# Optimization experiments

Hardware: AMD Instinct MI355X
Metric: run time of the kernel (lower is better)

Reference implementation:

```python
import jax, jax.numpy as jnp
import numpy as np

REG = 0.01
NUM_ITER = 5


def _l2norm(x):
    return x / jnp.linalg.norm(x, axis=-1, keepdims=True)


def setup_inputs() -> dict:
    key = jax.random.key(0)
    k1, k2 = jax.random.split(key)
    B, D = 8192, 256
    img = _l2norm(jax.random.normal(k1, (B, D), dtype=jnp.float32))
    # correlate text with image so diagonal similarity ~1 (CLIP-like), keeping
    # K = exp(-(1-sim)/0.01) numerically meaningful
    txt = _l2norm(img + 0.1 * jax.random.normal(k2, (B, D), dtype=jnp.float32))
    labels = jnp.arange(B, dtype=jnp.int64)
    logit_scale = jnp.float32(100.0)  # unused by the module, kept for signature
    return {"all_image_features": img, "all_text_features": txt,
            "logit_scale": logit_scale, "labels": labels}


def _sinkhorn_loss(M, labels, reg=REG, num_iter=NUM_ITER):
    n = M.shape[0]
    b_val = jnp.asarray(1.0 / n, M.dtype)  # b = [1/n, ...]; a = ones -> Kp = K
    u0 = jnp.ones((n,), M.dtype) / n
    v0 = jnp.ones((n,), M.dtype) / n
    K = jnp.exp(M / -reg)  # [n, n]

    def body(carry, _):
        u, v, done = carry
        KtU = K.T @ u                       # [n]
        v_new = b_val / KtU
        u_new = 1.0 / (K @ v_new)
        bad = (jnp.any(KtU == 0)
               | jnp.any(jnp.isnan(u_new)) | jnp.any(jnp.isnan(v_new))
               | jnp.any(jnp.isinf(u_new)) | jnp.any(jnp.isinf(v_new)))
        stop = done | bad  # torch version reverts to prev u,v and breaks
        u = jnp.where(stop, u, u_new)
        v = jnp.where(stop, v, v_new)
        return (u, v, stop), None

    (u, v, _), _ = jax.lax.scan(body, (u0, v0, jnp.bool_(False)), None, length=num_iter)
    P = u[:, None] * K * v[None, :]  # transport plan used as logits
    logp = jax.nn.log_softmax(P, axis=-1)
    return -jnp.mean(logp[jnp.arange(n), labels])


def reference(all_image_features, all_text_features, logit_scale, labels):
    logits_per_image = all_image_features @ all_text_features.T
    logits_per_text = all_text_features @ all_image_features.T
    loss = (_sinkhorn_loss(1.0 - logits_per_image, labels)
            + _sinkhorn_loss(1.0 - logits_per_text, labels)) / 2
    return loss
```

## Files before the change

kernel.cpp:

```cpp
#include <hip/hip_runtime.h>
#include <hip/hip_fp16.h>
#include <cstdint>
#include <cstddef>


#define N_DIM 8192
#define D_DIM 256
#define L2E100 144.26950408889634f
#define BVAL (1.0f / 8192.0f)
#define OCAP 4
#define NNZ_CAP (1u << 20)

typedef __attribute__((ext_vector_type(4))) float f32x4;
typedef __attribute__((ext_vector_type(8))) int i32x8;

__device__ __forceinline__ unsigned char f2bf8(float f) {
  union { __half h; unsigned short u; } x;
  x.h = __float2half(fminf(f, 57344.0f));
  unsigned short r = (unsigned short)(x.u + 0x7F + ((x.u >> 8) & 1));
  return (unsigned char)(r >> 8);
}
__device__ __forceinline__ float bf8tof(unsigned char b) {
  union { unsigned short u; __half h; } x; x.u = (unsigned short)((unsigned int)b << 8);
  return __half2float(x.h);
}
__device__ __forceinline__ unsigned int pack4_bf8(float a, float b, float c, float d) {
#if __has_builtin(__builtin_amdgcn_cvt_pk_bf8_f32)
  int u = 0;
  u = __builtin_amdgcn_cvt_pk_bf8_f32(a, b, u, false);
  u = __builtin_amdgcn_cvt_pk_bf8_f32(c, d, u, true);
  return (unsigned int)u;
#else
  return (unsigned int)f2bf8(a) | ((unsigned int)f2bf8(b) << 8) |
         ((unsigned int)f2bf8(c) << 16) | ((unsigned int)f2bf8(d) << 24);
#endif
}
__device__ __forceinline__ float frcp(float x) { return __builtin_amdgcn_rcpf(x); }

#define GLD_LDS16(g, l)                                                          \
  __builtin_amdgcn_global_load_lds(                                              \
      (const __attribute__((address_space(1))) unsigned int*)(g),                \
      (__attribute__((address_space(3))) unsigned int*)(l), 16, 0, 0)

__global__ __launch_bounds__(256) void cast_diag_kernel(const float* __restrict__ img,
                                                        const float* __restrict__ txt,
                                                        unsigned char* __restrict__ A8,
                                                        unsigned char* __restrict__ B8,
                                                        float* __restrict__ Ecol,
                                                        float* __restrict__ Thr,
                                                        float* __restrict__ Gdiag,
                                                        unsigned int* __restrict__ cnt,
                                                        float* __restrict__ out) {
  if (blockIdx.x == 0 && threadIdx.x == 0) { cnt[0] = 0u; out[0] = 0.0f; }
  const int t = threadIdx.x, lane = t & 63, wid = t >> 6;
  const int rowg = lane >> 4, seg = lane & 15;
  const int row = blockIdx.x * 16 + wid * 4 + rowg;
  const size_t base = (size_t)row * D_DIM + seg * 16;
  float av[16], bv[16];
  #pragma unroll
  for (int h = 0; h < 4; ++h) {
    float4 a4 = *reinterpret_cast<const float4*>(img + base + h * 4);
    float4 b4 = *reinterpret_cast<const float4*>(txt + base + h * 4);
    av[4*h] = a4.x; av[4*h+1] = a4.y; av[4*h+2] = a4.z; av[4*h+3] = a4.w;
    bv[4*h] = b4.x; bv[4*h+1] = b4.y; bv[4*h+2] = b4.z; bv[4*h+3] = b4.w;
  }
  float s = 0.0f;
  #pragma unroll
  for (int e = 0; e < 16; ++e) s += av[e] * bv[e];
  uint4 pa, pb;
  pa.x = pack4_bf8(av[0], av[1], av[2], av[3]);
  pa.y = pack4_bf8(av[4], av[5], av[6], av[7]);
  pa.z = pack4_bf8(av[8], av[9], av[10], av[11]);
  pa.w = pack4_bf8(av[12], av[13], av[14], av[15]);
  pb.x = pack4_bf8(bv[0], bv[1], bv[2], bv[3]);
  pb.y = pack4_bf8(bv[4], bv[5], bv[6], bv[7]);
  pb.z = pack4_bf8(bv[8], bv[9], bv[10], bv[11]);
  pb.w = pack4_bf8(bv[12], bv[13], bv[14], bv[15]);
  *reinterpret_cast<uint4*>(A8 + base) = pa;
  *reinterpret_cast<uint4*>(B8 + base) = pb;
  s += __shfl_xor(s, 1, 64); s += __shfl_xor(s, 2, 64);
  s += __shfl_xor(s, 4, 64); s += __shfl_xor(s, 8, 64);
  if (seg == 0) {
    const float E = rintf((1.0f - s) * L2E100);
    Ecol[row] = E;
    Thr[row] = (L2E100 - 19.5f - E) / L2E100;
    Gdiag[row] = bf8tof(f2bf8(exp2f(E - (1.0f - s) * L2E100)));
  }
}

__global__ __launch_bounds__(512, 4) void gemm_mx_sparse_kernel(
    const unsigned char* __restrict__ A8, const unsigned char* __restrict__ B8,
    const float* __restrict__ Ecol, const float* __restrict__ Thr,
    uint2* __restrict__ entries, unsigned int* __restrict__ cnt) {
  __shared__ __align__(16) char smem[65536];
  const int bid = blockIdx.x;
  const int sid = (bid & 7) * 512 + (bid >> 3);
  const int bi = sid >> 6, bj = sid & 63;
  const int t = threadIdx.x, lane = t & 63, wid = t >> 6;
  const int wr = wid >> 2, wc = wid & 3;
  const int al = lane & 15, kh = lane >> 4;
  const int xorv = al & 7;

  const int srow = t >> 3;
  const int sx = ((t & 7) ^ (srow & 7)) << 4;
  const unsigned char* Ab = A8 + (size_t)(bi * 128) * 256;
  const unsigned char* Bb = B8 + (size_t)(bj * 128) * 256;
  GLD_LDS16(Ab + (size_t)(srow)      * 256 + sx,       smem +         t * 16);
  GLD_LDS16(Ab + (size_t)(64 + srow) * 256 + sx,       smem +  8192 + t * 16);
  GLD_LDS16(Bb + (size_t)(srow)      * 256 + sx,       smem + 32768 + t * 16);
  GLD_LDS16(Bb + (size_t)(64 + srow) * 256 + sx,       smem + 40960 + t * 16);
  GLD_LDS16(Ab + (size_t)(srow)      * 256 + 128 + sx, smem + 16384 + t * 16);
  GLD_LDS16(Ab + (size_t)(64 + srow) * 256 + 128 + sx, smem + 24576 + t * 16);
  GLD_LDS16(Bb + (size_t)(srow)      * 256 + 128 + sx, smem + 49152 + t * 16);
  GLD_LDS16(Bb + (size_t)(64 + srow) * 256 + 128 + sx, smem + 57344 + t * 16);

  float4 th[4];
  #pragma unroll
  for (int m = 0; m < 4; ++m)
    th[m] = *reinterpret_cast<const float4*>(Thr + bi * 128 + wr * 64 + m * 16 + kh * 4);

  int offA[4], offB[2];
  #pragma unroll
  for (int m = 0; m < 4; ++m) offA[m] = (wr * 64 + m * 16 + al) * 128;
  #pragma unroll
  for (int n = 0; n < 2; ++n) offB[n] = 32768 + (wc * 32 + n * 16 + al) * 128;

  f32x4 acc[4][2] = {};

  #pragma unroll
  for (int ks = 0; ks < 2; ++ks) {
    if (ks == 0) {
      asm volatile("s_waitcnt vmcnt(4)" ::: "memory");
    } else {
      asm volatile("s_waitcnt vmcnt(0)" ::: "memory");
    }
    __builtin_amdgcn_sched_barrier(0);
    __builtin_amdgcn_s_barrier();
    __builtin_amdgcn_sched_barrier(0);

    const int kb = ks * 16384;
    const int b0 = ((kh * 2)     ^ xorv) << 4;
    const int b1 = ((kh * 2 + 1) ^ xorv) << 4;
    i32x8 av[4], bv[2];
    #pragma unroll
    for (int m = 0; m < 4; ++m) {
      int4 lo = *reinterpret_cast<const int4*>(smem + kb + offA[m] + b0);
      int4 hi = *reinterpret_cast<const int4*>(smem + kb + offA[m] + b1);
      av[m][0] = lo.x; av[m][1] = lo.y; av[m][2] = lo.z; av[m][3] = lo.w;
      av[m][4] = hi.x; av[m][5] = hi.y; av[m][6] = hi.z; av[m][7] = hi.w;
    }
    #pragma unroll
    for (int n = 0; n < 2; ++n) {
      int4 lo = *reinterpret_cast<const int4*>(smem + kb + offB[n] + b0);
      int4 hi = *reinterpret_cast<const int4*>(smem + kb + offB[n] + b1);
      bv[n][0] = lo.x; bv[n][1] = lo.y; bv[n][2] = lo.z; bv[n][3] = lo.w;
      bv[n][4] = hi.x; bv[n][5] = hi.y; bv[n][6] = hi.z; bv[n][7] = hi.w;
    }
    #pragma unroll
    for (int m = 0; m < 4; ++m)
      #pragma unroll
      for (int n = 0; n < 2; ++n)
        acc[m][n] = __builtin_amdgcn_mfma_scale_f32_16x16x128_f8f6f4(
            av[m], bv[n], acc[m][n],
            1, 1,
            0, 0x7F7F7F7F,
            0, 0x7F7F7F7F);
  }

  #pragma unroll
  for (int m = 0; m < 4; ++m) {
    const int ibase = bi * 128 + wr * 64 + m * 16 + kh * 4;
    #pragma unroll
    for (int n = 0; n < 2; ++n) {
      const bool hit = (acc[m][n][0] > th[m].x) | (acc[m][n][1] > th[m].y) |
                       (acc[m][n][2] > th[m].z) | (acc[m][n][3] > th[m].w);
      if (hit) {
        float4 e4 = *reinterpret_cast<const float4*>(Ecol + ibase);
        float x[4] = {fmaf(acc[m][n][0], L2E100, e4.x - L2E100),
                      fmaf(acc[m][n][1], L2E100, e4.y - L2E100),
                      fmaf(acc[m][n][2], L2E100, e4.z - L2E100),
                      fmaf(acc[m][n][3], L2E100, e4.w - L2E100)};
        unsigned int w = pack4_bf8(exp2f(fminf(x[0], 14.0f)), exp2f(fminf(x[1], 14.0f)),
                                   exp2f(fminf(x[2], 14.0f)), exp2f(fminf(x[3], 14.0f)));
        if (w != 0u) {
          const int jg = bj * 128 + wc * 32 + n * 16 + al;
          #pragma unroll
          for (int q = 0; q < 4; ++q) {
            unsigned int byte = (w >> (8 * q)) & 0xFFu;
            const int ig = ibase + q;
            if (byte && ig != jg) {
              unsigned int slot = atomicAdd(cnt, 1u);
              if (slot < NNZ_CAP)
                entries[slot] = make_uint2(((unsigned int)jg << 13) | (unsigned int)ig,
                                           __float_as_uint(bf8tof((unsigned char)byte)));
            }
          }
        }
      }
    }
  }
}

__global__ __launch_bounds__(1024) void sinkhorn_diag_kernel(
    const uint2* __restrict__ entries, const unsigned int* __restrict__ pCnt,
    const float* __restrict__ Gdiag, float2* __restrict__ tailScr,
    float* __restrict__ out) {
  const int t = threadIdx.x;
  const int i0 = t * 8;
  __shared__ float rowB[2][8192];
  __shared__ float colB[2][8192];
  const unsigned int raw = pCnt[0];
  const int noff = (int)(raw > NNZ_CAP ? NNZ_CAP : raw);

  if (noff == 0) {
    if (t == 0) out[0] = logf(8191.0f + 2.71828182845904523f) - 1.0f;
    return;
  }

  float gd[8];
  {
    float4 g0 = *reinterpret_cast<const float4*>(Gdiag + i0);
    float4 g1 = *reinterpret_cast<const float4*>(Gdiag + i0 + 4);
    gd[0] = g0.x; gd[1] = g0.y; gd[2] = g0.z; gd[3] = g0.w;
    gd[4] = g1.x; gd[5] = g1.y; gd[6] = g1.z; gd[7] = g1.w;
  }
  unsigned int erc[OCAP];
  float eg[OCAP];
  #pragma unroll
  for (int k = 0; k < OCAP; ++k) {
    const int e = t + k * 1024;
    if (e < noff) {
      uint2 en = entries[e];
      erc[k] = en.x; eg[k] = __uint_as_float(en.y);
    } else {
      erc[k] = 0u; eg[k] = 0.0f;
    }
  }
  const bool tail = noff > OCAP * 1024;

  #pragma unroll
  for (int p = 0; p < 10; ++p) {
    float* rowT = rowB[p & 1];
    float* colT = colB[p & 1];
    const float* rowS = rowB[(p + 1) & 1];
    const float* colS = colB[(p + 1) & 1];
    const float coeff = (p == 0 || (p & 1)) ? BVAL : 1.0f;
    #pragma unroll
    for (int h = 0; h < 2; ++h) {
      float4 rv, cv;
      if (p == 0) {
        rv = make_float4(gd[4 * h] * BVAL, gd[4 * h + 1] * BVAL,
                         gd[4 * h + 2] * BVAL, gd[4 * h + 3] * BVAL);
        cv = rv;
      } else {
        float4 cs = *reinterpret_cast<const float4*>(colS + i0 + 4 * h);
        float4 rs = *reinterpret_cast<const float4*>(rowS + i0 + 4 * h);
        rv = make_float4(gd[4 * h] * coeff * frcp(cs.x), gd[4 * h + 1] * coeff * frcp(cs.y),
                         gd[4 * h + 2] * coeff * frcp(cs.z), gd[4 * h + 3] * coeff * frcp(cs.w));
        cv = make_float4(gd[4 * h] * coeff * frcp(rs.x), gd[4 * h + 1] * coeff * frcp(rs.y),
                         gd[4 * h + 2] * coeff * frcp(rs.z), gd[4 * h + 3] * coeff * frcp(rs.w));
      }
      *reinterpret_cast<float4*>(rowT + i0 + 4 * h) = rv;
      *reinterpret_cast<float4*>(colT + i0 + 4 * h) = cv;
    }
    __syncthreads();
    #pragma unroll
    for (int k = 0; k < OCAP; ++k) {
      if (eg[k] != 0.0f) {
        const int r = (int)(erc[k] >> 13), c = (int)(erc[k] & 8191u);
        const float wcc = (p == 0) ? BVAL : coeff * frcp(colS[c]);
        const float wrr = (p == 0) ? BVAL : coeff * frcp(rowS[r]);
        atomicAdd(&rowT[r], eg[k] * wcc);
        atomicAdd(&colT[c], eg[k] * wrr);
      }
    }
    if (tail) {
      for (int e = OCAP * 1024 + t; e < noff; e += 1024) {
        uint2 en = entries[e];
        const int r = (int)(en.x >> 13), c = (int)(en.x & 8191u);
        const float g = __uint_as_float(en.y);
        const float wcc = (p == 0) ? BVAL : coeff * frcp(colS[c]);
        const float wrr = (p == 0) ? BVAL : coeff * frcp(rowS[r]);
        atomicAdd(&rowT[r], g * wcc);
        atomicAdd(&colT[c], g * wrr);
      }
    }
    __syncthreads();
  }

  const float* row9 = rowB[1]; const float* row8 = rowB[0];
  const float* col9 = colB[1]; const float* col8 = colB[0];

  float acc = 0.0f;
  float rE[8], cE[8];
  #pragma unroll
  for (int j = 0; j < 8; ++j) {
    const int i = i0 + j;
    const float u1 = frcp(row9[i]), v1 = BVAL * frcp(col8[i]);
    const float u2 = frcp(col9[i]), v2 = BVAL * frcp(row8[i]);
    const float p1 = u1 * gd[j] * v1, p2 = u2 * gd[j] * v2;
    acc -= p1 + p2;
    rE[j] = __expf(p1) - 1.0f;
    cE[j] = __expf(p2) - 1.0f;
  }
  float e1[OCAP], e2[OCAP];
  #pragma unroll
  for (int k = 0; k < OCAP; ++k) {
    if (eg[k] != 0.0f) {
      const int r = (int)(erc[k] >> 13), c = (int)(erc[k] & 8191u);
      e1[k] = __expf(frcp(row9[r]) * eg[k] * BVAL * frcp(col8[c])) - 1.0f;
      e2[k] = __expf(frcp(col9[c]) * eg[k] * BVAL * frcp(row8[r])) - 1.0f;
    } else { e1[k] = 0.0f; e2[k] = 0.0f; }
  }
  if (tail) {
    for (int e = OCAP * 1024 + t; e < noff; e += 1024) {
      uint2 en = entries[e];
      const int r = (int)(en.x >> 13), c = (int)(en.x & 8191u);
      const float g = __uint_as_float(en.y);
      tailScr[e - OCAP * 1024] =
          make_float2(__expf(frcp(row9[r]) * g * BVAL * frcp(col8[c])) - 1.0f,
                      __expf(frcp(col9[c]) * g * BVAL * frcp(row8[r])) - 1.0f);
    }
  }
  __syncthreads();

  float* rowE = rowB[0]; float* colE = colB[0];
  #pragma unroll
  for (int h = 0; h < 2; ++h) {
    *reinterpret_cast<float4*>(rowE + i0 + 4 * h) =
        make_float4(rE[4 * h], rE[4 * h + 1], rE[4 * h + 2], rE[4 * h + 3]);
    *reinterpret_cast<float4*>(colE + i0 + 4 * h) =
        make_float4(cE[4 * h], cE[4 * h + 1], cE[4 * h + 2], cE[4 * h + 3]);
  }
  __syncthreads();
  #pragma unroll
  for (int k = 0; k < OCAP; ++k) {
    if (eg[k] != 0.0f) {
      atomicAdd(&rowE[erc[k] >> 13], e1[k]);
      atomicAdd(&colE[erc[k] & 8191u], e2[k]);
    }
  }
  if (tail) {
    for (int e = OCAP * 1024 + t; e < noff; e += 1024) {
      unsigned int rc = entries[e].x;
      float2 ee = tailScr[e - OCAP * 1024];
      atomicAdd(&rowE[rc >> 13], ee.x);
      atomicAdd(&colE[rc & 8191u], ee.y);
    }
  }
  __syncthreads();

  #pragma unroll
  for (int j = 0; j < 8; ++j)
    acc += logf(8192.0f + rowE[i0 + j]) + logf(8192.0f + colE[i0 + j]);
  #pragma unroll
  for (int o = 32; o > 0; o >>= 1) acc += __shfl_down(acc, o, 64);
  __syncthreads();
  if ((t & 63) == 0) colB[1][t >> 6] = acc;
  __syncthreads();
  if (t == 0) {
    float s = 0.0f;
    #pragma unroll
    for (int w = 0; w < 16; ++w) s += colB[1][w];
    s *= 0.5f / 8192.0f;
    if (raw > NNZ_CAP) s = __int_as_float(0x7FC00000);
    out[0] = s;
  }
}

extern "C" void kernel_launch(void* const* d_in, const int* in_sizes, int n_in,
                              void* d_out, int out_size, void* d_ws, size_t ws_size,
                              hipStream_t stream) {
  const float* img = (const float*)d_in[0];
  const float* txt = (const float*)d_in[1];
  float* out = (float*)d_out;

  char* ws = (char*)d_ws;
  size_t off = 0;
  auto alloc = [&](size_t bytes) -> void* {
    void* p = ws + off;
    off += (bytes + 255) & ~(size_t)255;
    return p;
  };
  unsigned char* A8 = (unsigned char*)alloc((size_t)N_DIM * D_DIM);
  unsigned char* B8 = (unsigned char*)alloc((size_t)N_DIM * D_DIM);
  uint2* entries    = (uint2*)alloc((size_t)NNZ_CAP * 8);
  float2* tailScr   = (float2*)alloc((size_t)NNZ_CAP * 8);
  unsigned int* cnt = (unsigned int*)alloc(256);
  float* Ecol  = (float*)alloc(N_DIM * 4);
  float* Thr   = (float*)alloc(N_DIM * 4);
  float* Gdiag = (float*)alloc(N_DIM * 4);

  if (off > ws_size) {
    hipMemsetAsync(d_out, 0xFF, sizeof(float) * (out_size > 0 ? out_size : 1), stream);
    return;
  }

  cast_diag_kernel<<<512, 256, 0, stream>>>(img, txt, A8, B8, Ecol, Thr, Gdiag, cnt, out);
  gemm_mx_sparse_kernel<<<4096, 512, 0, stream>>>(A8, B8, Ecol, Thr, entries, cnt);
  sinkhorn_diag_kernel<<<1, 1024, 0, stream>>>(entries, cnt, Gdiag, tailScr, out);
}
```

Measured before the change: 48.41 us.

## Quantize features to FP4 and run the similarity GEMM with FP4 MFMA

Normalized features are now packed into FP4 (e2m1) nibbles with a fixed block scale of 2^-4 instead of bf8, which halves the operand bytes. The sparse-candidate GEMM uses the scaled MFMA in FP4 mode with 256-thread blocks, a 32KB LDS tile and a larger 64x64 per-wave output tile, loading all of K before one barrier. This cuts global and LDS traffic and the cost of the matrix instructions. The price is much coarser similarity values, so the threshold filter and off-diagonal kernel estimates may be less accurate.

New measurement: 39.83 us, median of 2. 17.7% less time.

```diff
diff --git a/kernel.cpp b/kernel.cpp
--- a/kernel.cpp
+++ b/kernel.cpp
@@ -35,6 +35,14 @@
          ((unsigned int)f2bf8(c) << 16) | ((unsigned int)f2bf8(d) << 24);
 #endif
 }
+__device__ __forceinline__ unsigned int fp4nib(float a) {
+  float v = fabsf(a) * 16.0f;
+  unsigned int s = (__float_as_uint(a) >> 31) << 3;
+  unsigned int c = (v < 0.25f) ? 0u : (v < 0.75f) ? 1u : (v < 1.25f) ? 2u
+                 : (v < 1.75f) ? 3u : (v < 2.5f)  ? 4u : (v < 3.5f)  ? 5u
+                 : (v < 5.0f)  ? 6u : 7u;
+  return s | c;
+}
 __device__ __forceinline__ float frcp(float x) { return __builtin_amdgcn_rcpf(x); }
 
 #define GLD_LDS16(g, l)                                                          \
@@ -44,8 +52,8 @@
 
 __global__ __launch_bounds__(256) void cast_diag_kernel(const float* __restrict__ img,
                                                         const float* __restrict__ txt,
-                                                        unsigned char* __restrict__ A8,
-                                                        unsigned char* __restrict__ B8,
+                                                        unsigned char* __restrict__ A4,
+                                                        unsigned char* __restrict__ B4,
                                                         float* __restrict__ Ecol,
                                                         float* __restrict__ Thr,
                                                         float* __restrict__ Gdiag,
@@ -67,17 +75,16 @@
   float s = 0.0f;
   #pragma unroll
   for (int e = 0; e < 16; ++e) s += av[e] * bv[e];
-  uint4 pa, pb;
-  pa.x = pack4_bf8(av[0], av[1], av[2], av[3]);
-  pa.y = pack4_bf8(av[4], av[5], av[6], av[7]);
-  pa.z = pack4_bf8(av[8], av[9], av[10], av[11]);
-  pa.w = pack4_bf8(av[12], av[13], av[14], av[15]);
-  pb.x = pack4_bf8(bv[0], bv[1], bv[2], bv[3]);
-  pb.y = pack4_bf8(bv[4], bv[5], bv[6], bv[7]);
-  pb.z = pack4_bf8(bv[8], bv[9], bv[10], bv[11]);
-  pb.w = pack4_bf8(bv[12], bv[13], bv[14], bv[15]);
-  *reinterpret_cast<uint4*>(A8 + base) = pa;
-  *reinterpret_cast<uint4*>(B8 + base) = pb;
+  unsigned int wa0 = 0, wa1 = 0, wb0 = 0, wb1 = 0;
+  #pragma unroll
+  for (int e = 0; e < 8; ++e) {
+    wa0 |= fp4nib(av[e]) << (4 * e);
+    wa1 |= fp4nib(av[8 + e]) << (4 * e);
+    wb0 |= fp4nib(bv[e]) << (4 * e);
+    wb1 |= fp4nib(bv[8 + e]) << (4 * e);
+  }
+  *reinterpret_cast<uint2*>(A4 + (size_t)row * 128 + seg * 8) = make_uint2(wa0, wa1);
+  *reinterpret_cast<uint2*>(B4 + (size_t)row * 128 + seg * 8) = make_uint2(wb0, wb1);
   s += __shfl_xor(s, 1, 64); s += __shfl_xor(s, 2, 64);
   s += __shfl_xor(s, 4, 64); s += __shfl_xor(s, 8, 64);
   if (seg == 0) {
@@ -88,90 +95,73 @@
   }
 }
 
-__global__ __launch_bounds__(512, 4) void gemm_mx_sparse_kernel(
-    const unsigned char* __restrict__ A8, const unsigned char* __restrict__ B8,
+__global__ __launch_bounds__(256, 4) void gemm_fp4_sparse_kernel(
+    const unsigned char* __restrict__ A4, const unsigned char* __restrict__ B4,
     const float* __restrict__ Ecol, const float* __restrict__ Thr,
     uint2* __restrict__ entries, unsigned int* __restrict__ cnt) {
-  __shared__ __align__(16) char smem[65536];
+  __shared__ __align__(16) char smem[32768];
   const int bid = blockIdx.x;
   const int sid = (bid & 7) * 512 + (bid >> 3);
   const int bi = sid >> 6, bj = sid & 63;
   const int t = threadIdx.x, lane = t & 63, wid = t >> 6;
-  const int wr = wid >> 2, wc = wid & 3;
+  const int wr = wid >> 1, wc = wid & 1;
   const int al = lane & 15, kh = lane >> 4;
-  const int xorv = al & 7;
-
-  const int srow = t >> 3;
-  const int sx = ((t & 7) ^ (srow & 7)) << 4;
-  const unsigned char* Ab = A8 + (size_t)(bi * 128) * 256;
-  const unsigned char* Bb = B8 + (size_t)(bj * 128) * 256;
-  GLD_LDS16(Ab + (size_t)(srow)      * 256 + sx,       smem +         t * 16);
-  GLD_LDS16(Ab + (size_t)(64 + srow) * 256 + sx,       smem +  8192 + t * 16);
-  GLD_LDS16(Bb + (size_t)(srow)      * 256 + sx,       smem + 32768 + t * 16);
-  GLD_LDS16(Bb + (size_t)(64 + srow) * 256 + sx,       smem + 40960 + t * 16);
-  GLD_LDS16(Ab + (size_t)(srow)      * 256 + 128 + sx, smem + 16384 + t * 16);
-  GLD_LDS16(Ab + (size_t)(64 + srow) * 256 + 128 + sx, smem + 24576 + t * 16);
-  GLD_LDS16(Bb + (size_t)(srow)      * 256 + 128 + sx, smem + 49152 + t * 16);
-  GLD_LDS16(Bb + (size_t)(64 + srow) * 256 + 128 + sx, smem + 57344 + t * 16);
+
+  const int srow = t >> 3, sp = t & 7;
+  const int sx = (sp ^ (srow & 7)) << 4;
+  const unsigned char* Ab = A4 + (size_t)(bi * 128) * 128;
+  const unsigned char* Bb = B4 + (size_t)(bj * 128) * 128;
+  #pragma unroll
+  for (int i = 0; i < 4; ++i)
+    GLD_LDS16(Ab + (size_t)(i * 32 + srow) * 128 + sx, smem + i * 4096 + t * 16);
+  #pragma unroll
+  for (int i = 0; i < 4; ++i)
+    GLD_LDS16(Bb + (size_t)(i * 32 + srow) * 128 + sx, smem + 16384 + i * 4096 + t * 16);
 
   float4 th[4];
   #pragma unroll
   for (int m = 0; m < 4; ++m)
     th[m] = *reinterpret_cast<const float4*>(Thr + bi * 128 + wr * 64 + m * 16 + kh * 4);
 
-  int offA[4], offB[2];
-  #pragma unroll
-  for (int m = 0; m < 4; ++m) offA[m] = (wr * 64 + m * 16 + al) * 128;
-  #pragma unroll
-  for (int n = 0; n < 2; ++n) offB[n] = 32768 + (wc * 32 + n * 16 + al) * 128;
-
-  f32x4 acc[4][2] = {};
+  f32x4 acc[4][4] = {};
+
+  asm volatile("s_waitcnt vmcnt(0)" ::: "memory");
+  __builtin_amdgcn_sched_barrier(0);
+  __builtin_amdgcn_s_barrier();
+  __builtin_amdgcn_sched_barrier(0);
 
   #pragma unroll
   for (int ks = 0; ks < 2; ++ks) {
-    if (ks == 0) {
-      asm volatile("s_waitcnt vmcnt(4)" ::: "memory");
-    } else {
-      asm volatile("s_waitcnt vmcnt(0)" ::: "memory");
-    }
-    __builtin_amdgcn_sched_barrier(0);
-    __builtin_amdgcn_s_barrier();
-    __builtin_amdgcn_sched_barrier(0);
-
-    const int kb = ks * 16384;
-    const int b0 = ((kh * 2)     ^ xorv) << 4;
-    const int b1 = ((kh * 2 + 1) ^ xorv) << 4;
-    i32x8 av[4], bv[2];
+    const int lb = ks * 4 + kh;
+    int4 ar[4];
     #pragma unroll
     for (int m = 0; m < 4; ++m) {
-      int4 lo = *reinterpret_cast<const int4*>(smem + kb + offA[m] + b0);
-      int4 hi = *reinterpret_cast<const int4*>(smem + kb + offA[m] + b1);
-      av[m][0] = lo.x; av[m][1] = lo.y; av[m][2] = lo.z; av[m][3] = lo.w;
-      av[m][4] = hi.x; av[m][5] = hi.y; av[m][6] = hi.z; av[m][7] = hi.w;
-    }
-    #pragma unroll
-    for (int n = 0; n < 2; ++n) {
-      int4 lo = *reinterpret_cast<const int4*>(smem + kb + offB[n] + b0);
-      int4 hi = *reinterpret_cast<const int4*>(smem + kb + offB[n] + b1);
-      bv[n][0] = lo.x; bv[n][1] = lo.y; bv[n][2] = lo.z; bv[n][3] = lo.w;
-      bv[n][4] = hi.x; bv[n][5] = hi.y; bv[n][6] = hi.z; bv[n][7] = hi.w;
-    }
-    #pragma unroll
-    for (int m = 0; m < 4; ++m)
+      const int row = wr * 64 + m * 16 + al;
+      ar[m] = *reinterpret_cast<const int4*>(smem + row * 128 + ((lb ^ (row & 7)) << 4));
+    }
+    #pragma unroll
+    for (int n = 0; n < 4; ++n) {
+      const int rowb = wc * 64 + n * 16 + al;
+      int4 br = *reinterpret_cast<const int4*>(smem + 16384 + rowb * 128 +
+                                               ((lb ^ (rowb & 7)) << 4));
+      i32x8 bvv = {br.x, br.y, br.z, br.w, 0, 0, 0, 0};
       #pragma unroll
-      for (int n = 0; n < 2; ++n)
+      for (int m = 0; m < 4; ++m) {
+        i32x8 avv = {ar[m].x, ar[m].y, ar[m].z, ar[m].w, 0, 0, 0, 0};
         acc[m][n] = __builtin_amdgcn_mfma_scale_f32_16x16x128_f8f6f4(
-            av[m], bv[n], acc[m][n],
-            1, 1,
-            0, 0x7F7F7F7F,
-            0, 0x7F7F7F7F);
+            avv, bvv, acc[m][n],
+            4, 4,
+            0, 0x7B7B7B7B,
+            0, 0x7B7B7B7B);
+      }
+    }
   }
 
   #pragma unroll
   for (int m = 0; m < 4; ++m) {
     const int ibase = bi * 128 + wr * 64 + m * 16 + kh * 4;
     #pragma unroll
-    for (int n = 0; n < 2; ++n) {
+    for (int n = 0; n < 4; ++n) {
       const bool hit = (acc[m][n][0] > th[m].x) | (acc[m][n][1] > th[m].y) |
                        (acc[m][n][2] > th[m].z) | (acc[m][n][3] > th[m].w);
       if (hit) {
@@ -183,7 +173,7 @@
         unsigned int w = pack4_bf8(exp2f(fminf(x[0], 14.0f)), exp2f(fminf(x[1], 14.0f)),
                                    exp2f(fminf(x[2], 14.0f)), exp2f(fminf(x[3], 14.0f)));
         if (w != 0u) {
-          const int jg = bj * 128 + wc * 32 + n * 16 + al;
+          const int jg = bj * 128 + wc * 64 + n * 16 + al;
           #pragma unroll
           for (int q = 0; q < 4; ++q) {
             unsigned int byte = (w >> (8 * q)) & 0xFFu;
@@ -382,8 +372,8 @@
     off += (bytes + 255) & ~(size_t)255;
     return p;
   };
-  unsigned char* A8 = (unsigned char*)alloc((size_t)N_DIM * D_DIM);
-  unsigned char* B8 = (unsigned char*)alloc((size_t)N_DIM * D_DIM);
+  unsigned char* A4 = (unsigned char*)alloc((size_t)N_DIM * 128);
+  unsigned char* B4 = (unsigned char*)alloc((size_t)N_DIM * 128);
   uint2* entries    = (uint2*)alloc((size_t)NNZ_CAP * 8);
   float2* tailScr   = (float2*)alloc((size_t)NNZ_CAP * 8);
   unsigned int* cnt = (unsigned int*)alloc(256);
@@ -396,7 +386,7 @@
     return;
   }
 
-  cast_diag_kernel<<<512, 256, 0, stream>>>(img, txt, A8, B8, Ecol, Thr, Gdiag, cnt, out);
-  gemm_mx_sparse_kernel<<<4096, 512, 0, stream>>>(A8, B8, Ecol, Thr, entries, cnt);
+  cast_diag_kernel<<<512, 256, 0, stream>>>(img, txt, A4, B4, Ecol, Thr, Gdiag, cnt, out);
+  gemm_fp4_sparse_kernel<<<4096, 256, 0, stream>>>(A4, B4, Ecol, Thr, entries, cnt);
   sinkhorn_diag_kernel<<<1, 1024, 0, stream>>>(entries, cnt, Gdiag, tailScr, out);
 }
```
